# Kernel optimization log

Hardware: AMD Instinct MI355X
Metric: run time of the kernel (lower is better)

The kernel has to match this reference:

```python
import jax, jax.numpy as jnp
import numpy as np

B, SQ, SK = 2, 2048, 2048
D, H = 1024, 16
HD = D // H              # head_dim = 64
R = 128                  # rel_pos_max_distance
P = 2 * R + 1            # num_pos_ids = 257
RADIUS = 256             # local_attention_radius


def setup_inputs() -> dict:
    key = jax.random.key(0)
    ks = jax.random.split(key, 8)
    s = 0.02
    return {
        "Q": jax.random.normal(ks[0], (B, SQ, D), dtype=jnp.float32),
        "K": jax.random.normal(ks[1], (B, SK, D), dtype=jnp.float32),
        "V": jax.random.normal(ks[2], (B, SK, D), dtype=jnp.float32),
        "Wq": jax.random.normal(ks[3], (D, D), dtype=jnp.float32) * s,
        "Wk": jax.random.normal(ks[4], (D, D), dtype=jnp.float32) * s,
        "Wv": jax.random.normal(ks[5], (D, D), dtype=jnp.float32) * s,
        "Wo": jax.random.normal(ks[6], (D, D), dtype=jnp.float32) * s,
        "E": jax.random.normal(ks[7], (P, D), dtype=jnp.float32) * s,  # rel_embeds
    }


def _split_heads(x, W):
    # bias-free projection then split: B x S x D -> B x H x S x HD
    y = x @ W.T
    b, s, _ = y.shape
    return y.reshape(b, s, H, HD).transpose(0, 2, 1, 3)


def reference(Q, K, V, Wq, Wk, Wv, Wo, E):
    q = _split_heads(Q, Wq)  # B,H,Sq,HD
    k = _split_heads(K, Wk)  # B,H,Sk,HD
    v = _split_heads(V, Wv)  # B,H,Sk,HD

    # rel_embeds reshape matches torch: E[p] viewed as (head_dim, num_heads)
    rel = E.reshape(P, HD, H).transpose(2, 0, 1)           # H,P,HD
    Q_rel = jnp.einsum("bhqd,hpd->bhqp", q, rel)           # B,H,Sq,P

    # slided relative position ids: clip(j - i, -R, R) + R
    i = jnp.arange(SQ)[:, None]
    j = jnp.arange(SK)[None, :]
    rel_ids = jnp.clip(j - i, -R, R) + R                   # Sq,Sk
    rel_shift = jnp.take_along_axis(
        Q_rel, jnp.broadcast_to(rel_ids, (B, H, SQ, SK)), axis=3
    )                                                       # B,H,Sq,Sk

    energy = (jnp.einsum("bhqd,bhkd->bhqk", q, k) + rel_shift) / jnp.sqrt(
        jnp.float32(HD)
    )

    # local attention mask: True = masked (outside window of radius RADIUS)
    mask = jnp.abs(j - i) > RADIUS                          # Sq,Sk
    mask = mask & ~jnp.all(mask, axis=-1, keepdims=True)    # never mask full rows
    energy = jnp.where(mask[None, None], -jnp.inf, energy)

    attn = jax.nn.softmax(energy, axis=-1)                  # B,H,Sq,Sk
    out = jnp.einsum("bhqk,bhkd->bhqd", attn, v)            # B,H,Sq,HD
    # torch: view(B,H,Sq,HD).permute(0,2,3,1).flatten(2,3) -> B,Sq,(HD*H)
    out = out.transpose(0, 2, 3, 1).reshape(B, SQ, D)
    return out @ Wo.T
```

## Files before the change

### kernel.cpp

```cpp
#include <hip/hip_runtime.h>
#include <hip/hip_bf16.h>

#define BATCH 2
#define SQn 2048
#define SKn 2048
#define DMODEL 1024
#define NH 16
#define HD 64
#define NPOS 257
#define RWIN 128
#define RADIUS 256

typedef __attribute__((ext_vector_type(8))) short bf16x8;
typedef __attribute__((ext_vector_type(4))) float f32x4;

static __device__ __forceinline__ unsigned short f2bf(float f) {
    union { float f; unsigned u; } v; v.f = f;
    unsigned r = (v.u + 0x7FFFu + ((v.u >> 16) & 1u)) >> 16;
    return (unsigned short)r;
}
static __device__ __forceinline__ float bf2f(unsigned short b) {
    union { unsigned u; float f; } v; v.u = ((unsigned)b) << 16;
    return v.f;
}

static __device__ __forceinline__ void gl_lds16(const unsigned short* g, unsigned short* l) {
    __builtin_amdgcn_global_load_lds(
        (const __attribute__((address_space(1))) unsigned*)g,
        (__attribute__((address_space(3))) unsigned*)l, 16, 0, 0);
}

__global__ __launch_bounds__(256) void convert_kernel(
    const float* __restrict__ Q, const float* __restrict__ K, const float* __restrict__ V,
    const float* __restrict__ Wq, const float* __restrict__ Wk, const float* __restrict__ Wv,
    const float* __restrict__ Wo,
    unsigned short* __restrict__ xb,
    unsigned short* __restrict__ wb,
    unsigned short* __restrict__ woh)
{
    int i = blockIdx.x * 256 + threadIdx.x;
    if (i < 3145728) {
        int which = i >> 20;
        int off = i & 1048575;
        const float* src = which == 0 ? Q : (which == 1 ? K : V);
        unsigned short* dst = xb + (size_t)which * 4194304;
        float4 v4 = ((const float4*)src)[off];
        ushort4 o4;
        o4.x = f2bf(v4.x); o4.y = f2bf(v4.y); o4.z = f2bf(v4.z); o4.w = f2bf(v4.w);
        ((ushort4*)dst)[off] = o4;
    } else {
        int i2 = i - 3145728;
        int which = i2 >> 18;
        int off = i2 & 262143;
        if (which < 3) {
            const float* src = which == 0 ? Wq : (which == 1 ? Wk : Wv);
            unsigned short* dst = wb + (size_t)which * 1048576;
            float4 v4 = ((const float4*)src)[off];
            ushort4 o4;
            o4.x = f2bf(v4.x); o4.y = f2bf(v4.y); o4.z = f2bf(v4.z); o4.w = f2bf(v4.w);
            ((ushort4*)dst)[off] = o4;
        } else {
            float4 v4 = ((const float4*)Wo)[off];
            int e0 = off * 4;
            int n  = e0 >> 10;
            int c0 = e0 & 1023;
            int d  = c0 >> 4;
            int h0 = c0 & 15;
            woh[((size_t)(h0 + 0) * 1024 + n) * 64 + d] = f2bf(v4.x);
            woh[((size_t)(h0 + 1) * 1024 + n) * 64 + d] = f2bf(v4.y);
            woh[((size_t)(h0 + 2) * 1024 + n) * 64 + d] = f2bf(v4.z);
            woh[((size_t)(h0 + 3) * 1024 + n) * 64 + d] = f2bf(v4.w);
        }
    }
}

__global__ __launch_bounds__(256) void mfma_gemm(
    const unsigned short* __restrict__ Xall,
    const unsigned short* __restrict__ Wall,
    unsigned short* __restrict__ Yall)
{
    __shared__ unsigned short S[16384];

    const int tid  = threadIdx.x;
    const int wv   = tid >> 6;
    const int lane = tid & 63;
    const int quad = lane >> 4;
    const int l15  = lane & 15;
    const int z    = blockIdx.z;
    const int m0   = blockIdx.x * 128;
    const int n0   = blockIdx.y * 128;
    const int wr   = (wv >> 1) * 64;
    const int wc   = (wv & 1) * 64;

    const unsigned short* X = Xall + (size_t)z * (4096 * 1024);
    const unsigned short* W = Wall + (size_t)z * (1024 * 1024);

    int srow[2], scol[2];
#pragma unroll
    for (int it = 0; it < 2; ++it) {
        int f = it * 256 + tid;
        srow[it] = f >> 2;
        scol[it] = ((f & 3) ^ ((srow[it] >> 1) & 3)) * 8;
    }

    int aoff[4], boff[4];
#pragma unroll
    for (int t = 0; t < 4; ++t) {
        int R = wr + t * 16 + l15;
        aoff[t] = R * 32 + ((quad ^ ((R >> 1) & 3)) * 8);
        int C = wc + t * 16 + l15;
        boff[t] = C * 32 + ((quad ^ ((C >> 1) & 3)) * 8);
    }

    f32x4 acc[4][4];
#pragma unroll
    for (int i = 0; i < 4; ++i)
#pragma unroll
        for (int j = 0; j < 4; ++j)
            acc[i][j] = (f32x4){0.f, 0.f, 0.f, 0.f};

#pragma unroll
    for (int it = 0; it < 2; ++it) {
        int f = it * 256 + tid;
        gl_lds16(X + (size_t)(m0 + srow[it]) * 1024 + scol[it], &S[f * 8]);
        gl_lds16(W + (size_t)(n0 + srow[it]) * 1024 + scol[it], &S[8192 + f * 8]);
    }

    for (int k0 = 0; k0 < 1024; k0 += 32) {
        const int cur = (k0 >> 5) & 1;
        __syncthreads();

        if (k0 + 32 < 1024) {
            const int nxt = cur ^ 1;
            const int kn = k0 + 32;
#pragma unroll
            for (int it = 0; it < 2; ++it) {
                int f = it * 256 + tid;
                gl_lds16(X + (size_t)(m0 + srow[it]) * 1024 + kn + scol[it],
                         &S[nxt * 4096 + f * 8]);
                gl_lds16(W + (size_t)(n0 + srow[it]) * 1024 + kn + scol[it],
                         &S[8192 + nxt * 4096 + f * 8]);
            }
        }

        const unsigned short* bA = &S[cur * 4096];
        const unsigned short* bB = &S[8192 + cur * 4096];
        bf16x8 a[4], b[4];
#pragma unroll
        for (int t = 0; t < 4; ++t) a[t] = *(const bf16x8*)&bA[aoff[t]];
#pragma unroll
        for (int t = 0; t < 4; ++t) b[t] = *(const bf16x8*)&bB[boff[t]];
#pragma unroll
        for (int i = 0; i < 4; ++i)
#pragma unroll
            for (int j = 0; j < 4; ++j)
                acc[i][j] = __builtin_amdgcn_mfma_f32_16x16x32_bf16(a[i], b[j], acc[i][j], 0, 0, 0);
    }

    unsigned short* Y = Yall + (size_t)z * (4096 * 1024);
    const int b_ = m0 >> 11;
    const int s0 = m0 & (SQn - 1);

    if (z < 2) {
#pragma unroll
        for (int i = 0; i < 4; ++i) {
            int mbase = s0 + wr + i * 16 + quad * 4;
#pragma unroll
            for (int j = 0; j < 4; ++j) {
                int col = n0 + wc + j * 16 + l15;
                int h = col >> 6, dd = col & 63;
                unsigned short* yb = Y + (((size_t)(b_ * NH + h) * SQn) << 6) + dd;
#pragma unroll
                for (int r = 0; r < 4; ++r)
                    yb[(size_t)(mbase + r) << 6] = f2bf(acc[i][j][r]);
            }
        }
    } else {
        unsigned short* const sT = S;
#pragma unroll
        for (int hh = 0; hh < 2; ++hh) {
            __syncthreads();
            if ((wv & 1) == hh) {
#pragma unroll
                for (int i = 0; i < 4; ++i) {
                    int mloc = wr + i * 16 + quad * 4;
#pragma unroll
                    for (int j = 0; j < 4; ++j) {
                        ushort4 pk;
                        pk.x = f2bf(acc[i][j][0]);
                        pk.y = f2bf(acc[i][j][1]);
                        pk.z = f2bf(acc[i][j][2]);
                        pk.w = f2bf(acc[i][j][3]);
                        *(ushort4*)&sT[(j * 16 + l15) * 136 + mloc] = pk;
                    }
                }
            }
            __syncthreads();
            int h = (n0 >> 6) + hh;
            unsigned short* yb = Y + ((size_t)(b_ * NH + h) * HD) * SKn + s0;
#pragma unroll
            for (int it = 0; it < 4; ++it) {
                int u = it * 256 + tid;
                int dd = u >> 4, mc = u & 15;
                uint4 val = *(const uint4*)&sT[dd * 136 + mc * 8];
                *(uint4*)(yb + (size_t)dd * SKn + mc * 8) = val;
            }
        }
    }
}

__global__ __launch_bounds__(256) void gemm_out(
    const unsigned short* __restrict__ aoh,
    const unsigned short* __restrict__ woh,
    float* __restrict__ Y)
{
    __shared__ unsigned short S[24576];

    const int tid  = threadIdx.x;
    const int wv   = tid >> 6;
    const int lane = tid & 63;
    const int quad = lane >> 4;
    const int l15  = lane & 15;
    const int m0   = blockIdx.x * 64;
    const int n0   = blockIdx.y * 128;
    const int wr   = (wv >> 1) * 32;
    const int wc   = (wv & 1) * 64;
    const int b_   = m0 >> 11;
    const int s0   = m0 & (SQn - 1);

    int rowa[2], ca[2];
#pragma unroll
    for (int it = 0; it < 2; ++it) {
        int f = it * 256 + tid;
        rowa[it] = f >> 3;
        ca[it]   = ((f & 7) ^ (rowa[it] & 7)) * 8;
    }
    int rowb[4], cb[4];
#pragma unroll
    for (int it = 0; it < 4; ++it) {
        int f = it * 256 + tid;
        rowb[it] = f >> 3;
        cb[it]   = ((f & 7) ^ (rowb[it] & 7)) * 8;
    }

    int aoff[2][2], boff[2][4];
#pragma unroll
    for (int ks = 0; ks < 2; ++ks) {
#pragma unroll
        for (int i = 0; i < 2; ++i) {
            int R = wr + i * 16 + l15;
            aoff[ks][i] = R * 64 + ((((ks << 2) + quad) ^ (R & 7)) * 8);
        }
#pragma unroll
        for (int j = 0; j < 4; ++j) {
            int C = wc + j * 16 + l15;
            boff[ks][j] = C * 64 + ((((ks << 2) + quad) ^ (C & 7)) * 8);
        }
    }

    f32x4 acc[2][4];
#pragma unroll
    for (int i = 0; i < 2; ++i)
#pragma unroll
        for (int j = 0; j < 4; ++j)
            acc[i][j] = (f32x4){0.f, 0.f, 0.f, 0.f};

    {
        const unsigned short* Ah = aoh + ((size_t)(b_ * NH) * SQn + s0) * HD;
        const unsigned short* Bh = woh + (size_t)n0 * HD;
#pragma unroll
        for (int it = 0; it < 2; ++it)
            gl_lds16(Ah + (size_t)rowa[it] * HD + ca[it], &S[(it * 256 + tid) * 8]);
#pragma unroll
        for (int it = 0; it < 4; ++it)
            gl_lds16(Bh + (size_t)rowb[it] * HD + cb[it], &S[8192 + (it * 256 + tid) * 8]);
    }

    for (int h = 0; h < NH; ++h) {
        const int cur = h & 1;
        __syncthreads();

        if (h + 1 < NH) {
            const int nxt = cur ^ 1;
            const unsigned short* Ah = aoh + ((size_t)(b_ * NH + h + 1) * SQn + s0) * HD;
            const unsigned short* Bh = woh + ((size_t)(h + 1) * 1024 + n0) * HD;
#pragma unroll
            for (int it = 0; it < 2; ++it)
                gl_lds16(Ah + (size_t)rowa[it] * HD + ca[it],
                         &S[nxt * 4096 + (it * 256 + tid) * 8]);
#pragma unroll
            for (int it = 0; it < 4; ++it)
                gl_lds16(Bh + (size_t)rowb[it] * HD + cb[it],
                         &S[8192 + nxt * 8192 + (it * 256 + tid) * 8]);
        }

        const unsigned short* bA = &S[cur * 4096];
        const unsigned short* bB = &S[8192 + cur * 8192];

        bf16x8 a0[2], b0[4];
#pragma unroll
        for (int i = 0; i < 2; ++i) a0[i] = *(const bf16x8*)&bA[aoff[0][i]];
#pragma unroll
        for (int j = 0; j < 4; ++j) b0[j] = *(const bf16x8*)&bB[boff[0][j]];
#pragma unroll
        for (int i = 0; i < 2; ++i)
#pragma unroll
            for (int j = 0; j < 4; ++j)
                acc[i][j] = __builtin_amdgcn_mfma_f32_16x16x32_bf16(a0[i], b0[j], acc[i][j], 0, 0, 0);

        bf16x8 a1[2], b1[4];
#pragma unroll
        for (int i = 0; i < 2; ++i) a1[i] = *(const bf16x8*)&bA[aoff[1][i]];
#pragma unroll
        for (int j = 0; j < 4; ++j) b1[j] = *(const bf16x8*)&bB[boff[1][j]];
#pragma unroll
        for (int i = 0; i < 2; ++i)
#pragma unroll
            for (int j = 0; j < 4; ++j)
                acc[i][j] = __builtin_amdgcn_mfma_f32_16x16x32_bf16(a1[i], b1[j], acc[i][j], 0, 0, 0);
    }

#pragma unroll
    for (int i = 0; i < 2; ++i) {
        int mbase = m0 + wr + i * 16 + quad * 4;
#pragma unroll
        for (int j = 0; j < 4; ++j) {
            int col = n0 + wc + j * 16 + l15;
#pragma unroll
            for (int r = 0; r < 4; ++r)
                Y[(size_t)(mbase + r) * DMODEL + col] = acc[i][j][r];
        }
    }
}

__global__ __launch_bounds__(256) void relt_kernel(
    const float* __restrict__ E, unsigned short* __restrict__ relTb)
{
    int idx = blockIdx.x * 256 + threadIdx.x;
    const int total = NH * NPOS * HD;
    if (idx < total) {
        int d = idx & (HD - 1);
        int p = (idx >> 6) % NPOS;
        int h = idx / (NPOS * HD);
        relTb[idx] = f2bf(E[(size_t)p * DMODEL + d * NH + h]);
    }
}

#define BIAS_S2 0.0014089565402528222f
#define SC2     0.1803368801111204f

__global__ __launch_bounds__(256, 2) void attn_mfma(
    const unsigned short* __restrict__ q,
    const unsigned short* __restrict__ k,
    const unsigned short* __restrict__ vT,
    const unsigned short* __restrict__ relTb,
    unsigned short* __restrict__ aoh)
{
    __shared__ unsigned short sK[64 * 64];
    __shared__ unsigned short sVt[64 * 64];
    __shared__ unsigned short sP[4][16 * 72];
    __shared__ signed char    sq8[128 * 260];
    unsigned short* const sQ = (unsigned short*)sq8;

    const int tid  = threadIdx.x;
    const int w    = tid >> 6;
    const int lane = tid & 63;
    const int quad = lane >> 4;
    const int l15  = lane & 15;
    const int xcd  = blockIdx.x & 7;
    const int sidx = blockIdx.x >> 3;
    const int bh   = (xcd << 2) | (sidx >> 4);
    const int q0   = (sidx & 15) << 7;
    const int h    = bh & (NH - 1);

    const int f1 = tid,       row1 = f1 >> 3;
    const int c1 = ((f1 & 7) ^ (row1 & 7)) * 8;
    const int f2 = 256 + tid, row2 = f2 >> 3;
    const int c2 = ((f2 & 7) ^ (row2 & 7)) * 8;

    {
        const unsigned short* gq = q + ((size_t)bh * SQn + q0) * HD;
#pragma unroll
        for (int it = 0; it < 4; ++it) {
            int f = it * 256 + tid;
            int row = f >> 3;
            int c = ((f & 7) ^ (row & 7)) * 8;
            gl_lds16(gq + row * HD + c, &sQ[f * 8]);
        }
    }
    __syncthreads();

    const int qrow = w * 16 + l15;
    const int qs = (quad ^ (qrow & 7)) * 8;
    bf16x8 a0A = *(const bf16x8*)&sQ[qrow * 64 + qs];
    bf16x8 a1A = *(const bf16x8*)&sQ[qrow * 64 + (qs ^ 32)];
    bf16x8 a0B = *(const bf16x8*)&sQ[(64 + qrow) * 64 + qs];
    bf16x8 a1B = *(const bf16x8*)&sQ[(64 + qrow) * 64 + (qs ^ 32)];

    const int myrow = w * 16 + quad * 4;
    for (int c5 = 0; c5 < 5; ++c5) {
        __syncthreads();
        const unsigned short* gr = relTb + ((size_t)h * NPOS + c5 * 64) * HD;
        gl_lds16(gr + row1 * HD + c1, &sK[f1 * 8]);
        gl_lds16(gr + row2 * HD + c2, &sK[f2 * 8]);
        __syncthreads();
#pragma unroll
        for (int t = 0; t < 4; ++t) {
            int prow = t * 16 + l15;
            int ks = (quad ^ (prow & 7)) * 8;
            bf16x8 b0 = *(const bf16x8*)&sK[prow * 64 + ks];
            bf16x8 b1 = *(const bf16x8*)&sK[prow * 64 + (ks ^ 32)];
            f32x4 ccA = {0.f, 0.f, 0.f, 0.f};
            ccA = __builtin_amdgcn_mfma_f32_16x16x32_bf16(a0A, b0, ccA, 0, 0, 0);
            ccA = __builtin_amdgcn_mfma_f32_16x16x32_bf16(a1A, b1, ccA, 0, 0, 0);
            f32x4 ccB = {0.f, 0.f, 0.f, 0.f};
            ccB = __builtin_amdgcn_mfma_f32_16x16x32_bf16(a0B, b0, ccB, 0, 0, 0);
            ccB = __builtin_amdgcn_mfma_f32_16x16x32_bf16(a1B, b1, ccB, 0, 0, 0);
            int pos = c5 * 64 + t * 16 + l15;
            if (pos < NPOS) {
#pragma unroll
                for (int r = 0; r < 4; ++r) {
                    int iqA = (int)rintf(ccA[r] * 128.0f);
                    iqA = iqA < -127 ? -127 : (iqA > 127 ? 127 : iqA);
                    sq8[(myrow + r) * 260 + pos] = (signed char)iqA;
                    int iqB = (int)rintf(ccB[r] * 128.0f);
                    iqB = iqB < -127 ? -127 : (iqB > 127 ? 127 : iqB);
                    sq8[(64 + myrow + r) * 260 + pos] = (signed char)iqB;
                }
            }
        }
    }
    __syncthreads();

    float bias0A[4], bias256A[4], bias0B[4], bias256B[4];
#pragma unroll
    for (int r = 0; r < 4; ++r) {
        bias0A[r]   = (float)sq8[(myrow + r) * 260 + 0]          * BIAS_S2;
        bias256A[r] = (float)sq8[(myrow + r) * 260 + 256]        * BIAS_S2;
        bias0B[r]   = (float)sq8[(64 + myrow + r) * 260 + 0]     * BIAS_S2;
        bias256B[r] = (float)sq8[(64 + myrow + r) * 260 + 256]   * BIAS_S2;
    }

    const int lo = (q0 - RADIUS) > 0 ? (q0 - RADIUS) : 0;
    const int hi = (q0 + 127 + RADIUS) < (SKn - 1) ? (q0 + 127 + RADIUS) : (SKn - 1);
    const int nt = ((hi - lo) >> 6) + 1;
    const int e_ = l15 - quad * 4;

    const unsigned short* kg = k  + (size_t)bh * SKn * HD;
    const unsigned short* vg = vT + (size_t)bh * HD * SKn;

    float laccA[4] = {0.f, 0.f, 0.f, 0.f};
    float laccB[4] = {0.f, 0.f, 0.f, 0.f};
    f32x4 oA[4], oB[4];
#pragma unroll
    for (int t = 0; t < 4; ++t) {
        oA[t] = (f32x4){0.f, 0.f, 0.f, 0.f};
        oB[t] = (f32x4){0.f, 0.f, 0.f, 0.f};
    }

    {
        gl_lds16(kg + (size_t)(lo + row1) * HD + c1, &sK[f1 * 8]);
        gl_lds16(kg + (size_t)(lo + row2) * HD + c2, &sK[f2 * 8]);
        gl_lds16(vg + (size_t)row1 * SKn + lo + c1, &sVt[f1 * 8]);
        gl_lds16(vg + (size_t)row2 * SKn + lo + c2, &sVt[f2 * 8]);
    }

    for (int kt = 0; kt < nt; ++kt) {
        const int kb = lo + (kt << 6);
        __syncthreads();

        bf16x8 kf0[4], kf1[4], vf0[4], vf1[4];
#pragma unroll
        for (int t = 0; t < 4; ++t) {
            int prow = t * 16 + l15;
            int ks = (quad ^ (prow & 7)) * 8;
            kf0[t] = *(const bf16x8*)&sK[prow * 64 + ks];
            kf1[t] = *(const bf16x8*)&sK[prow * 64 + (ks ^ 32)];
            vf0[t] = *(const bf16x8*)&sVt[prow * 64 + ks];
            vf1[t] = *(const bf16x8*)&sVt[prow * 64 + (ks ^ 32)];
        }
        __syncthreads();

        if (kt + 1 < nt) {
            const int kb2 = kb + 64;
            gl_lds16(kg + (size_t)(kb2 + row1) * HD + c1, &sK[f1 * 8]);
            gl_lds16(kg + (size_t)(kb2 + row2) * HD + c2, &sK[f2 * 8]);
            gl_lds16(vg + (size_t)row1 * SKn + kb2 + c1, &sVt[f1 * 8]);
            gl_lds16(vg + (size_t)row2 * SKn + kb2 + c2, &sVt[f2 * 8]);
        }

        const int dtbaseA = kb - q0 - w * 16;
        if (dtbaseA > -320 && dtbaseA < 272) {
#pragma unroll
            for (int t = 0; t < 4; ++t) {
                const int dt = dtbaseA + t * 16;
                const int spb = (quad * 4) * 72 + t * 16 + l15;
                if (dt <= -272 || dt >= 272) {
#pragma unroll
                    for (int r = 0; r < 4; ++r) sP[w][spb + r * 72] = 0;
                } else {
                    f32x4 sc = {0.f, 0.f, 0.f, 0.f};
                    sc = __builtin_amdgcn_mfma_f32_16x16x32_bf16(a0A, kf0[t], sc, 0, 0, 0);
                    sc = __builtin_amdgcn_mfma_f32_16x16x32_bf16(a1A, kf1[t], sc, 0, 0, 0);

                    float pv[4];
                    if (dt >= -112 && dt <= 112) {
                        int idx0 = myrow * 260 + dt + 128 + e_;
#pragma unroll
                        for (int r = 0; r < 4; ++r) {
                            float bf = (float)sq8[idx0 + r * 259] * BIAS_S2;
                            pv[r] = __builtin_amdgcn_exp2f(fmaf(sc[r], SC2, bf));
                        }
                    } else if (dt >= -240 && dt <= -144) {
#pragma unroll
                        for (int r = 0; r < 4; ++r)
                            pv[r] = __builtin_amdgcn_exp2f(fmaf(sc[r], SC2, bias0A[r]));
                    } else if (dt >= 144 && dt <= 240) {
#pragma unroll
                        for (int r = 0; r < 4; ++r)
                            pv[r] = __builtin_amdgcn_exp2f(fmaf(sc[r], SC2, bias256A[r]));
                    } else {
#pragma unroll
                        for (int r = 0; r < 4; ++r) {
                            int d = dt + e_ - r;
                            bool in = (unsigned)(d + RADIUS) <= 2u * RADIUS;
                            int p = d < -RWIN ? 0 : (d > RWIN ? 2 * RWIN : d + RWIN);
                            float bf = (float)sq8[(myrow + r) * 260 + p] * BIAS_S2;
                            float e = __builtin_amdgcn_exp2f(fmaf(sc[r], SC2, bf));
                            pv[r] = in ? e : 0.0f;
                        }
                    }
#pragma unroll
                    for (int r = 0; r < 4; ++r) {
                        unsigned short pb = f2bf(pv[r]);
                        sP[w][spb + r * 72] = pb;
                        laccA[r] += bf2f(pb);
                    }
                }
            }
            bf16x8 p0 = *(const bf16x8*)&sP[w][l15 * 72 + quad * 8];
            bf16x8 p1 = *(const bf16x8*)&sP[w][l15 * 72 + 32 + quad * 8];
#pragma unroll
            for (int t = 0; t < 4; ++t) {
                oA[t] = __builtin_amdgcn_mfma_f32_16x16x32_bf16(p0, vf0[t], oA[t], 0, 0, 0);
                oA[t] = __builtin_amdgcn_mfma_f32_16x16x32_bf16(p1, vf1[t], oA[t], 0, 0, 0);
            }
        }

        const int dtbaseB = dtbaseA - 64;
        if (dtbaseB > -320 && dtbaseB < 272) {
#pragma unroll
            for (int t = 0; t < 4; ++t) {
                const int dt = dtbaseB + t * 16;
                const int spb = (quad * 4) * 72 + t * 16 + l15;
                if (dt <= -272 || dt >= 272) {
#pragma unroll
                    for (int r = 0; r < 4; ++r) sP[w][spb + r * 72] = 0;
                } else {
                    f32x4 sc = {0.f, 0.f, 0.f, 0.f};
                    sc = __builtin_amdgcn_mfma_f32_16x16x32_bf16(a0B, kf0[t], sc, 0, 0, 0);
                    sc = __builtin_amdgcn_mfma_f32_16x16x32_bf16(a1B, kf1[t], sc, 0, 0, 0);

                    float pv[4];
                    if (dt >= -112 && dt <= 112) {
                        int idx0 = (64 + myrow) * 260 + dt + 128 + e_;
#pragma unroll
                        for (int r = 0; r < 4; ++r) {
                            float bf = (float)sq8[idx0 + r * 259] * BIAS_S2;
                            pv[r] = __builtin_amdgcn_exp2f(fmaf(sc[r], SC2, bf));
                        }
                    } else if (dt >= -240 && dt <= -144) {
#pragma unroll
                        for (int r = 0; r < 4; ++r)
                            pv[r] = __builtin_amdgcn_exp2f(fmaf(sc[r], SC2, bias0B[r]));
                    } else if (dt >= 144 && dt <= 240) {
#pragma unroll
                        for (int r = 0; r < 4; ++r)
                            pv[r] = __builtin_amdgcn_exp2f(fmaf(sc[r], SC2, bias256B[r]));
                    } else {
#pragma unroll
                        for (int r = 0; r < 4; ++r) {
                            int d = dt + e_ - r;
                            bool in = (unsigned)(d + RADIUS) <= 2u * RADIUS;
                            int p = d < -RWIN ? 0 : (d > RWIN ? 2 * RWIN : d + RWIN);
                            float bf = (float)sq8[(64 + myrow + r) * 260 + p] * BIAS_S2;
                            float e = __builtin_amdgcn_exp2f(fmaf(sc[r], SC2, bf));
                            pv[r] = in ? e : 0.0f;
                        }
                    }
#pragma unroll
                    for (int r = 0; r < 4; ++r) {
                        unsigned short pb = f2bf(pv[r]);
                        sP[w][spb + r * 72] = pb;
                        laccB[r] += bf2f(pb);
                    }
                }
            }
            bf16x8 p0 = *(const bf16x8*)&sP[w][l15 * 72 + quad * 8];
            bf16x8 p1 = *(const bf16x8*)&sP[w][l15 * 72 + 32 + quad * 8];
#pragma unroll
            for (int t = 0; t < 4; ++t) {
                oB[t] = __builtin_amdgcn_mfma_f32_16x16x32_bf16(p0, vf0[t], oB[t], 0, 0, 0);
                oB[t] = __builtin_amdgcn_mfma_f32_16x16x32_bf16(p1, vf1[t], oB[t], 0, 0, 0);
            }
        }
    }

    float linvA[4], linvB[4];
#pragma unroll
    for (int r = 0; r < 4; ++r) {
        float lA = laccA[r];
        float lB = laccB[r];
#pragma unroll
        for (int off = 1; off <= 8; off <<= 1) {
            lA += __shfl_xor(lA, off);
            lB += __shfl_xor(lB, off);
        }
        linvA[r] = 1.0f / lA;
        linvB[r] = 1.0f / lB;
    }

    unsigned short* ob = aoh + ((size_t)bh * SQn + q0) * HD;
#pragma unroll
    for (int t = 0; t < 4; ++t) {
#pragma unroll
        for (int r = 0; r < 4; ++r) {
            int irow = w * 16 + quad * 4 + r;
            ob[irow * HD + t * 16 + l15] = f2bf(oA[t][r] * linvA[r]);
            ob[(64 + irow) * HD + t * 16 + l15] = f2bf(oB[t][r] * linvB[r]);
        }
    }
}

extern "C" void kernel_launch(void* const* d_in, const int* in_sizes, int n_in,
                              void* d_out, int out_size, void* d_ws, size_t ws_size,
                              hipStream_t stream) {
    const float* Q  = (const float*)d_in[0];
    const float* K  = (const float*)d_in[1];
    const float* V  = (const float*)d_in[2];
    const float* Wq = (const float*)d_in[3];
    const float* Wk = (const float*)d_in[4];
    const float* Wv = (const float*)d_in[5];
    const float* Wo = (const float*)d_in[6];
    const float* E  = (const float*)d_in[7];
    float* out = (float*)d_out;

    char* p = (char*)d_ws;
    unsigned short* xb    = (unsigned short*)p; p += (size_t)24 << 20;
    unsigned short* wb    = (unsigned short*)p; p += (size_t)6  << 20;
    unsigned short* woh   = (unsigned short*)p; p += (size_t)2  << 20;
    unsigned short* head  = (unsigned short*)p; p += (size_t)24 << 20;
    unsigned short* relTb = (unsigned short*)p; p += (size_t)1  << 20;
    unsigned short* aoh   = (unsigned short*)p;

    unsigned short* qb  = head;
    unsigned short* kb  = head + 4194304;
    unsigned short* vTb = head + 8388608;

    dim3 bb(256);
    convert_kernel<<<dim3(16384), bb, 0, stream>>>(Q, K, V, Wq, Wk, Wv, Wo, xb, wb, woh);
    relt_kernel<<<dim3(1028), bb, 0, stream>>>(E, relTb);
    mfma_gemm<<<dim3(32, 8, 3), bb, 0, stream>>>(xb, wb, head);
    attn_mfma<<<dim3(BATCH * NH * (SQn / 128)), bb, 0, stream>>>(qb, kb, vTb, relTb, aoh);
    gemm_out<<<dim3(64, 8), bb, 0, stream>>>(aoh, woh, out);
}
```

Baseline: 208.8 us.

## Shrink QKV GEMM tile to 64x128 and remap blocks for XCD locality

```diff
diff --git a/kernel.cpp b/kernel.cpp
--- a/kernel.cpp
+++ b/kernel.cpp
@@ -74,56 +74,68 @@
     }
 }
 
-__global__ __launch_bounds__(256) void mfma_gemm(
+__global__ __launch_bounds__(256, 6) void mfma_gemm(
     const unsigned short* __restrict__ Xall,
     const unsigned short* __restrict__ Wall,
     unsigned short* __restrict__ Yall)
 {
-    __shared__ unsigned short S[16384];
+    __shared__ unsigned short S[12288];
 
     const int tid  = threadIdx.x;
     const int wv   = tid >> 6;
     const int lane = tid & 63;
     const int quad = lane >> 4;
     const int l15  = lane & 15;
-    const int z    = blockIdx.z;
-    const int m0   = blockIdx.x * 128;
-    const int n0   = blockIdx.y * 128;
-    const int wr   = (wv >> 1) * 64;
+
+    const int lin  = blockIdx.x;
+    const int nl   = (lin & 7) * 192 + (lin >> 3);
+    const int mt   = nl & 63;
+    const int rest = nl >> 6;
+    const int nt   = rest & 7;
+    const int z    = rest >> 3;
+    const int m0   = mt * 64;
+    const int n0   = nt * 128;
+    const int wr   = (wv >> 1) * 32;
     const int wc   = (wv & 1) * 64;
 
     const unsigned short* X = Xall + (size_t)z * (4096 * 1024);
     const unsigned short* W = Wall + (size_t)z * (1024 * 1024);
 
-    int srow[2], scol[2];
+    const int arow = tid >> 2;
+    const int acol = ((tid & 3) ^ ((arow >> 1) & 3)) * 8;
+    int brow[2], bcol[2];
 #pragma unroll
     for (int it = 0; it < 2; ++it) {
         int f = it * 256 + tid;
-        srow[it] = f >> 2;
-        scol[it] = ((f & 3) ^ ((srow[it] >> 1) & 3)) * 8;
-    }
-
-    int aoff[4], boff[4];
-#pragma unroll
-    for (int t = 0; t < 4; ++t) {
-        int R = wr + t * 16 + l15;
-        aoff[t] = R * 32 + ((quad ^ ((R >> 1) & 3)) * 8);
-        int C = wc + t * 16 + l15;
-        boff[t] = C * 32 + ((quad ^ ((C >> 1) & 3)) * 8);
-    }
-
-    f32x4 acc[4][4];
-#pragma unroll
-    for (int i = 0; i < 4; ++i)
+        brow[it] = f >> 2;
+        bcol[it] = ((f & 3) ^ ((brow[it] >> 1) & 3)) * 8;
+    }
+
+    int aoff[2], boff[4];
+#pragma unroll
+    for (int i = 0; i < 2; ++i) {
+        int R = wr + i * 16 + l15;
+        aoff[i] = R * 32 + ((quad ^ ((R >> 1) & 3)) * 8);
+    }
+#pragma unroll
+    for (int j = 0; j < 4; ++j) {
+        int C = wc + j * 16 + l15;
+        boff[j] = C * 32 + ((quad ^ ((C >> 1) & 3)) * 8);
+    }
+
+    f32x4 acc[2][4];
+#pragma unroll
+    for (int i = 0; i < 2; ++i)
 #pragma unroll
         for (int j = 0; j < 4; ++j)
             acc[i][j] = (f32x4){0.f, 0.f, 0.f, 0.f};
 
-#pragma unroll
-    for (int it = 0; it < 2; ++it) {
-        int f = it * 256 + tid;
-        gl_lds16(X + (size_t)(m0 + srow[it]) * 1024 + scol[it], &S[f * 8]);
-        gl_lds16(W + (size_t)(n0 + srow[it]) * 1024 + scol[it], &S[8192 + f * 8]);
+    {
+        gl_lds16(X + (size_t)(m0 + arow) * 1024 + acol, &S[tid * 8]);
+#pragma unroll
+        for (int it = 0; it < 2; ++it)
+            gl_lds16(W + (size_t)(n0 + brow[it]) * 1024 + bcol[it],
+                     &S[4096 + (it * 256 + tid) * 8]);
     }
 
     for (int k0 = 0; k0 < 1024; k0 += 32) {
@@ -133,25 +145,23 @@
         if (k0 + 32 < 1024) {
             const int nxt = cur ^ 1;
             const int kn = k0 + 32;
-#pragma unroll
-            for (int it = 0; it < 2; ++it) {
-                int f = it * 256 + tid;
-                gl_lds16(X + (size_t)(m0 + srow[it]) * 1024 + kn + scol[it],
-                         &S[nxt * 4096 + f * 8]);
-                gl_lds16(W + (size_t)(n0 + srow[it]) * 1024 + kn + scol[it],
-                         &S[8192 + nxt * 4096 + f * 8]);
-            }
-        }
-
-        const unsigned short* bA = &S[cur * 4096];
-        const unsigned short* bB = &S[8192 + cur * 4096];
-        bf16x8 a[4], b[4];
-#pragma unroll
-        for (int t = 0; t < 4; ++t) a[t] = *(const bf16x8*)&bA[aoff[t]];
-#pragma unroll
-        for (int t = 0; t < 4; ++t) b[t] = *(const bf16x8*)&bB[boff[t]];
-#pragma unroll
-        for (int i = 0; i < 4; ++i)
+            gl_lds16(X + (size_t)(m0 + arow) * 1024 + kn + acol,
+                     &S[nxt * 2048 + tid * 8]);
+#pragma unroll
+            for (int it = 0; it < 2; ++it)
+                gl_lds16(W + (size_t)(n0 + brow[it]) * 1024 + kn + bcol[it],
+                         &S[4096 + nxt * 4096 + (it * 256 + tid) * 8]);
+        }
+
+        const unsigned short* bA = &S[cur * 2048];
+        const unsigned short* bB = &S[4096 + cur * 4096];
+        bf16x8 a[2], b[4];
+#pragma unroll
+        for (int i = 0; i < 2; ++i) a[i] = *(const bf16x8*)&bA[aoff[i]];
+#pragma unroll
+        for (int j = 0; j < 4; ++j) b[j] = *(const bf16x8*)&bB[boff[j]];
+#pragma unroll
+        for (int i = 0; i < 2; ++i)
 #pragma unroll
             for (int j = 0; j < 4; ++j)
                 acc[i][j] = __builtin_amdgcn_mfma_f32_16x16x32_bf16(a[i], b[j], acc[i][j], 0, 0, 0);
@@ -163,7 +173,7 @@
 
     if (z < 2) {
 #pragma unroll
-        for (int i = 0; i < 4; ++i) {
+        for (int i = 0; i < 2; ++i) {
             int mbase = s0 + wr + i * 16 + quad * 4;
 #pragma unroll
             for (int j = 0; j < 4; ++j) {
@@ -182,7 +192,7 @@
             __syncthreads();
             if ((wv & 1) == hh) {
 #pragma unroll
-                for (int i = 0; i < 4; ++i) {
+                for (int i = 0; i < 2; ++i) {
                     int mloc = wr + i * 16 + quad * 4;
 #pragma unroll
                     for (int j = 0; j < 4; ++j) {
@@ -191,7 +201,7 @@
                         pk.y = f2bf(acc[i][j][1]);
                         pk.z = f2bf(acc[i][j][2]);
                         pk.w = f2bf(acc[i][j][3]);
-                        *(ushort4*)&sT[(j * 16 + l15) * 136 + mloc] = pk;
+                        *(ushort4*)&sT[(j * 16 + l15) * 72 + mloc] = pk;
                     }
                 }
             }
@@ -199,11 +209,11 @@
             int h = (n0 >> 6) + hh;
             unsigned short* yb = Y + ((size_t)(b_ * NH + h) * HD) * SKn + s0;
 #pragma unroll
-            for (int it = 0; it < 4; ++it) {
+            for (int it = 0; it < 2; ++it) {
                 int u = it * 256 + tid;
-                int dd = u >> 4, mc = u & 15;
-                uint4 val = *(const uint4*)&sT[dd * 136 + mc * 8];
-                *(uint4*)(yb + (size_t)dd * SKn + mc * 8) = val;
+                int dd = u >> 3, mc = (u & 7) * 8;
+                uint4 val = *(const uint4*)&sT[dd * 72 + mc];
+                *(uint4*)(yb + (size_t)dd * SKn + mc) = val;
             }
         }
     }
@@ -660,7 +670,7 @@
     dim3 bb(256);
     convert_kernel<<<dim3(16384), bb, 0, stream>>>(Q, K, V, Wq, Wk, Wv, Wo, xb, wb, woh);
     relt_kernel<<<dim3(1028), bb, 0, stream>>>(E, relTb);
-    mfma_gemm<<<dim3(32, 8, 3), bb, 0, stream>>>(xb, wb, head);
+    mfma_gemm<<<dim3(1536), bb, 0, stream>>>(xb, wb, head);
     attn_mfma<<<dim3(BATCH * NH * (SQn / 128)), bb, 0, stream>>>(qb, kb, vTb, relTb, aoh);
     gemm_out<<<dim3(64, 8), bb, 0, stream>>>(aoh, woh, out);
 }
```

Result: no change. 207.3 us (-0.7%).
